# Optimization experiments

Hardware: AMD Instinct MI355X
Metric: run time of the kernel (lower is better)

## Reference

```python
import jax, jax.numpy as jnp
import numpy as np

B, S, D = 2, 2048, 2048
H, HD, RD = 16, 128, 64
ND = HD - RD  # nope head dim = 64
QR, KVR = 1536, 512  # q/kv lora ranks
EPS = 1e-6


def rmsnorm(x, w):
    return x * jax.lax.rsqrt(jnp.mean(x * x, axis=-1, keepdims=True) + EPS) * w


def rope_rotate(x, cos, sin):
    # x: [B, h, S, r]; cos/sin: [S, r/2]; pairwise complex rotation
    xr, xi = x[..., 0::2], x[..., 1::2]
    o_r = xr * cos - xi * sin
    o_i = xr * sin + xi * cos
    return jnp.stack([o_r, o_i], axis=-1).reshape(x.shape)


def setup_inputs() -> dict:
    key = jax.random.key(0)
    ks = jax.random.split(key, 12)
    sd = 0.02
    # rotary tables for rope_head_dim
    inv_freq = 1.0 / (10000.0 ** (np.arange(0, RD, 2, dtype=np.float32) / RD))
    t = np.arange(S, dtype=np.float32)
    ang = np.outer(t, inv_freq)  # [S, RD/2]
    return {
        "x": jax.random.normal(ks[0], (B, S, D), dtype=jnp.float32),
        "freqs_cos": jnp.asarray(np.cos(ang)),
        "freqs_sin": jnp.asarray(np.sin(ang)),
        "w_cq": jax.random.normal(ks[1], (QR, D), dtype=jnp.float32) * sd,
        "w_dq_nope": jax.random.normal(ks[2], (H * ND, QR), dtype=jnp.float32) * sd,
        "w_dq_rope": jax.random.normal(ks[3], (H * RD, QR), dtype=jnp.float32) * sd,
        "w_ckv": jax.random.normal(ks[4], (KVR, D), dtype=jnp.float32) * sd,
        "w_dk_nope": jax.random.normal(ks[5], (H * ND, KVR), dtype=jnp.float32) * sd,
        "w_dv": jax.random.normal(ks[6], (H * HD, KVR), dtype=jnp.float32) * sd,
        "w_krope": jax.random.normal(ks[7], (RD, D), dtype=jnp.float32) * sd,
        "w_proj": jax.random.normal(ks[8], (H * HD, H * HD), dtype=jnp.float32) * sd,
        "q_norm_w": jnp.ones((QR,), dtype=jnp.float32),
        "kv_norm_w": jnp.ones((KVR,), dtype=jnp.float32),
    }


def reference(x, freqs_cos, freqs_sin, w_cq, w_dq_nope, w_dq_rope, w_ckv,
              w_dk_nope, w_dv, w_krope, w_proj, q_norm_w, kv_norm_w):
    b, s, _ = x.shape
    # low-rank q path
    norm_q = rmsnorm(jnp.einsum("bsd,rd->bsr", x, w_cq), q_norm_w)
    q_nope = jnp.einsum("bsr,or->bso", norm_q, w_dq_nope).reshape(b, s, H, ND).transpose(0, 2, 1, 3)
    q_rope = jnp.einsum("bsr,or->bso", norm_q, w_dq_rope).reshape(b, s, H, RD).transpose(0, 2, 1, 3)
    # low-rank kv path
    norm_kv = rmsnorm(jnp.einsum("bsd,rd->bsr", x, w_ckv), kv_norm_w)
    k_nope = jnp.einsum("bsr,or->bso", norm_kv, w_dk_nope).reshape(b, s, H, ND).transpose(0, 2, 1, 3)
    v = jnp.einsum("bsr,or->bso", norm_kv, w_dv).reshape(b, s, H, HD).transpose(0, 2, 1, 3)
    # shared single-head rope key from x directly
    k_rope_raw = jnp.einsum("bsd,rd->bsr", x, w_krope).reshape(b, s, 1, RD).transpose(0, 2, 1, 3)
    # NOTE: source does `k_rope, q_rope = apply_rope(query_rope, key_rope, cis)`,
    # i.e. the rotated query lands in the K slot and the rotated (1-head) key in the Q slot.
    k_rope = rope_rotate(q_rope, freqs_cos, freqs_sin)            # [B,H,S,RD]
    q_rope_out = rope_rotate(k_rope_raw, freqs_cos, freqs_sin)     # [B,1,S,RD]
    q = jnp.concatenate([q_nope, jnp.broadcast_to(q_rope_out, (b, H, s, RD))], axis=-1)
    k = jnp.concatenate([k_nope, k_rope], axis=-1)
    # causal SDPA, scale 1/sqrt(head_dim)
    scores = jnp.einsum("bhqd,bhkd->bhqk", q, k) / jnp.sqrt(jnp.float32(HD))
    mask = jnp.tril(jnp.ones((s, s), dtype=bool))
    scores = jnp.where(mask, scores, jnp.finfo(scores.dtype).min)
    attn = jax.nn.softmax(scores, axis=-1)
    out = jnp.einsum("bhqk,bhkd->bhqd", attn, v)  # [B,H,S,HD]
    out = out.transpose(0, 2, 1, 3).reshape(b, s, H * HD)
    return jnp.einsum("bso,po->bsp", out, w_proj)
```

## Files before the change

kernel.cpp:

```cpp
#include <hip/hip_runtime.h>

typedef __attribute__((ext_vector_type(4))) float f32x4;
typedef __attribute__((ext_vector_type(8))) short short8;
typedef unsigned short ushort_t;

__device__ __forceinline__ float bf2f(ushort_t u) {
  unsigned int i = ((unsigned int)u) << 16;
  return __builtin_bit_cast(float, i);
}
__device__ __forceinline__ ushort_t f2bf(float f) {
  unsigned int x = __builtin_bit_cast(unsigned int, f);
  unsigned int r = (x + 0x7FFFu + ((x >> 16) & 1u)) >> 16;
  return (ushort_t)r;
}

__global__ __launch_bounds__(256)
void cvt_all(const float* __restrict__ x, const float* __restrict__ wcq,
             const float* __restrict__ wdqn, const float* __restrict__ wdqr,
             const float* __restrict__ wckv, const float* __restrict__ wdkn,
             const float* __restrict__ wdv, const float* __restrict__ wkr,
             const float* __restrict__ wpr,
             ushort_t* ox, ushort_t* owcq, ushort_t* owdqn, ushort_t* owdqr,
             ushort_t* owckv, ushort_t* owdkn, ushort_t* owdv, ushort_t* owkr,
             ushort_t* owpr) {
  int bid = blockIdx.x;
  const float* in; ushort_t* out;
  if (bid < 8192)       { in = x;    out = ox;    }
  else if (bid < 11264) { in = wcq;  out = owcq;  bid -= 8192;  }
  else if (bid < 12800) { in = wdqn; out = owdqn; bid -= 11264; }
  else if (bid < 14336) { in = wdqr; out = owdqr; bid -= 12800; }
  else if (bid < 15360) { in = wckv; out = owckv; bid -= 14336; }
  else if (bid < 15872) { in = wdkn; out = owdkn; bid -= 15360; }
  else if (bid < 16896) { in = wdv;  out = owdv;  bid -= 15872; }
  else if (bid < 17024) { in = wkr;  out = owkr;  bid -= 16896; }
  else                  { in = wpr;  out = owpr;  bid -= 17024; }
  const long i = ((long)bid * 256 + threadIdx.x) * 4;
  float4 v = *(const float4*)(in + i);
  ushort4 o;
  o.x = f2bf(v.x); o.y = f2bf(v.y); o.z = f2bf(v.z); o.w = f2bf(v.w);
  *(ushort4*)(out + i) = o;
}

template <int OUT_BF16>
__global__ __launch_bounds__(256)
void gemm_bt(const ushort_t* __restrict__ A, const ushort_t* __restrict__ B,
             void* __restrict__ Cv, int M, int N, int K) {
  __shared__ __align__(16) ushort_t As[128 * 64];
  __shared__ __align__(16) ushort_t Bs[128 * 64];
  const int tid = threadIdx.x;
  const int lane = tid & 63;
  const int wid = tid >> 6;
  const int m0 = blockIdx.y * 128;
  const int n0 = blockIdx.x * 128;
  const int wm = (wid >> 1) * 64;
  const int wn = (wid & 1) * 64;

  f32x4 acc[4][4];
#pragma unroll
  for (int m = 0; m < 4; ++m)
#pragma unroll
    for (int n = 0; n < 4; ++n) acc[m][n] = (f32x4){0.f, 0.f, 0.f, 0.f};

  const int ktiles = K >> 6;
  for (int kt = 0; kt < ktiles; ++kt) {
    const int k0 = kt << 6;
    __syncthreads();
#pragma unroll
    for (int i = 0; i < 4; ++i) {
      const int chunk = (i * 4 + wid) * 1024;
      const int o = chunk + lane * 16;
      const int row = o >> 7;
      const int cb = o & 127;
      const ushort_t* src = A + (long)(m0 + row) * K + (k0 + (cb >> 1));
      __builtin_amdgcn_global_load_lds((const __attribute__((address_space(1))) unsigned int*)src,
                                       (__attribute__((address_space(3))) unsigned int*)((char*)As + chunk),
                                       16, 0, 0);
    }
#pragma unroll
    for (int i = 0; i < 4; ++i) {
      const int chunk = (i * 4 + wid) * 1024;
      const int o = chunk + lane * 16;
      const int row = o >> 7;
      const int cb = o & 127;
      int brow = n0 + row;
      if (brow > N - 1) brow = N - 1;
      const ushort_t* src = B + (long)brow * K + (k0 + (cb >> 1));
      __builtin_amdgcn_global_load_lds((const __attribute__((address_space(1))) unsigned int*)src,
                                       (__attribute__((address_space(3))) unsigned int*)((char*)Bs + chunk),
                                       16, 0, 0);
    }
    __syncthreads();
#pragma unroll
    for (int kk = 0; kk < 2; ++kk) {
      const int kb = kk * 32 + ((lane >> 4) << 3);
      short8 a[4], b[4];
#pragma unroll
      for (int m = 0; m < 4; ++m)
        a[m] = *(const short8*)(As + (wm + m * 16 + (lane & 15)) * 64 + kb);
#pragma unroll
      for (int n = 0; n < 4; ++n)
        b[n] = *(const short8*)(Bs + (wn + n * 16 + (lane & 15)) * 64 + kb);
#pragma unroll
      for (int m = 0; m < 4; ++m)
#pragma unroll
        for (int n = 0; n < 4; ++n)
          acc[m][n] = __builtin_amdgcn_mfma_f32_16x16x32_bf16(a[m], b[n], acc[m][n], 0, 0, 0);
    }
  }
  const int rb = m0 + wm + ((lane >> 4) << 2);
  const int cbase = n0 + wn + (lane & 15);
#pragma unroll
  for (int m = 0; m < 4; ++m)
#pragma unroll
    for (int n = 0; n < 4; ++n) {
      const int c = cbase + n * 16;
      if (c < N) {
#pragma unroll
        for (int j = 0; j < 4; ++j) {
          const long r = rb + m * 16 + j;
          if (OUT_BF16)
            ((ushort_t*)Cv)[r * N + c] = f2bf(acc[m][n][j]);
          else
            ((float*)Cv)[r * N + c] = acc[m][n][j];
        }
      }
    }
}

__global__ __launch_bounds__(256)
void gemm_bt3(const ushort_t* __restrict__ A,
              const ushort_t* __restrict__ B0, ushort_t* __restrict__ C0, int nb0, int N0,
              const ushort_t* __restrict__ B1, ushort_t* __restrict__ C1, int nb1, int N1,
              const ushort_t* __restrict__ B2, ushort_t* __restrict__ C2, int N2,
              int K, int tvSeg) {
  __shared__ __align__(16) ushort_t S[16384];
  ushort_t* As = S;
  ushort_t* Bs = S + 8192;
  int bx = blockIdx.x;
  const ushort_t* Bp; ushort_t* Cp; int N; int seg;
  if (bx < nb0)            { Bp = B0; Cp = C0; N = N0; seg = 0; }
  else if (bx < nb0 + nb1) { Bp = B1; Cp = C1; N = N1; seg = 1; bx -= nb0; }
  else                     { Bp = B2; Cp = C2; N = N2; seg = 2; bx -= nb0 + nb1; }
  const int tid = threadIdx.x;
  const int lane = tid & 63;
  const int wid = tid >> 6;
  const int m0 = blockIdx.y * 128;
  const int n0 = bx * 128;
  const int wm = (wid >> 1) * 64;
  const int wn = (wid & 1) * 64;

  f32x4 acc[4][4];
#pragma unroll
  for (int m = 0; m < 4; ++m)
#pragma unroll
    for (int n = 0; n < 4; ++n) acc[m][n] = (f32x4){0.f, 0.f, 0.f, 0.f};

  const int ktiles = K >> 6;
  for (int kt = 0; kt < ktiles; ++kt) {
    const int k0 = kt << 6;
    __syncthreads();
#pragma unroll
    for (int i = 0; i < 4; ++i) {
      const int chunk = (i * 4 + wid) * 1024;
      const int o = chunk + lane * 16;
      const int row = o >> 7;
      const int cb = o & 127;
      const ushort_t* src = A + (long)(m0 + row) * K + (k0 + (cb >> 1));
      __builtin_amdgcn_global_load_lds((const __attribute__((address_space(1))) unsigned int*)src,
                                       (__attribute__((address_space(3))) unsigned int*)((char*)As + chunk),
                                       16, 0, 0);
    }
#pragma unroll
    for (int i = 0; i < 4; ++i) {
      const int chunk = (i * 4 + wid) * 1024;
      const int o = chunk + lane * 16;
      const int row = o >> 7;
      const int cb = o & 127;
      int brow = n0 + row;
      if (brow > N - 1) brow = N - 1;
      const ushort_t* src = Bp + (long)brow * K + (k0 + (cb >> 1));
      __builtin_amdgcn_global_load_lds((const __attribute__((address_space(1))) unsigned int*)src,
                                       (__attribute__((address_space(3))) unsigned int*)((char*)Bs + chunk),
                                       16, 0, 0);
    }
    __syncthreads();
#pragma unroll
    for (int kk = 0; kk < 2; ++kk) {
      const int kb = kk * 32 + ((lane >> 4) << 3);
      short8 a[4], b[4];
#pragma unroll
      for (int m = 0; m < 4; ++m)
        a[m] = *(const short8*)(As + (wm + m * 16 + (lane & 15)) * 64 + kb);
#pragma unroll
      for (int n = 0; n < 4; ++n)
        b[n] = *(const short8*)(Bs + (wn + n * 16 + (lane & 15)) * 64 + kb);
#pragma unroll
      for (int m = 0; m < 4; ++m)
#pragma unroll
        for (int n = 0; n < 4; ++n)
          acc[m][n] = __builtin_amdgcn_mfma_f32_16x16x32_bf16(a[m], b[n], acc[m][n], 0, 0, 0);
    }
  }
  if (seg == tvSeg) {
    __syncthreads();
    const int lrb = wm + ((lane >> 4) << 2);
    const int ldb = wn + (lane & 15);
#pragma unroll
    for (int m = 0; m < 4; ++m)
#pragma unroll
      for (int n = 0; n < 4; ++n) {
        const int ld = ldb + n * 16;
#pragma unroll
        for (int j = 0; j < 4; ++j) {
          const int lr = lrb + m * 16 + j;
          *(ushort_t*)((char*)S + lr * 256 + ((2 * ld) ^ ((lr & 15) << 4))) = f2bf(acc[m][n][j]);
        }
      }
    __syncthreads();
    const int b = m0 >> 11;
    const int s0 = m0 & 2047;
    const int bh = b * 16 + bx;
    const int d = tid & 127;
    const int sh = (tid >> 7) * 64;
#pragma unroll
    for (int i = 0; i < 8; ++i) {
      const int sbase = sh + i * 8;
      short8 val;
#pragma unroll
      for (int j = 0; j < 8; ++j) {
        const int s = sbase + j;
        val[j] = (short)*(const ushort_t*)((const char*)S + s * 256 + ((2 * d) ^ ((s & 15) << 4)));
      }
      *(short8*)(Cp + ((long)bh * 128 + d) * 2048 + s0 + sbase) = val;
    }
    return;
  }
  const int rb = m0 + wm + ((lane >> 4) << 2);
  const int cbase = n0 + wn + (lane & 15);
#pragma unroll
  for (int m = 0; m < 4; ++m)
#pragma unroll
    for (int n = 0; n < 4; ++n) {
      const int c = cbase + n * 16;
      if (c < N) {
#pragma unroll
        for (int j = 0; j < 4; ++j) {
          const long r = rb + m * 16 + j;
          Cp[r * N + c] = f2bf(acc[m][n][j]);
        }
      }
    }
}

__device__ __forceinline__ void rms_body(const ushort_t* x, const float* w,
                                         ushort_t* out, int R, float* warr) {
  const int tid = threadIdx.x;
  float ss = 0.f;
  for (int i = tid; i < R; i += 256) { float v = bf2f(x[i]); ss += v * v; }
#pragma unroll
  for (int off = 32; off; off >>= 1) ss += __shfl_xor(ss, off);
  if ((tid & 63) == 0) warr[tid >> 6] = ss;
  __syncthreads();
  const float tot = warr[0] + warr[1] + warr[2] + warr[3];
  const float rs = rsqrtf(tot / (float)R + 1e-6f);
  for (int i = tid; i < R; i += 256) out[i] = f2bf(bf2f(x[i]) * rs * w[i]);
}

__global__ __launch_bounds__(256)
void rmsnorm_both(const ushort_t* __restrict__ ckv, const float* __restrict__ kvnw,
                  ushort_t* __restrict__ nkv,
                  const ushort_t* __restrict__ cq, const float* __restrict__ qnw,
                  ushort_t* __restrict__ nq) {
  __shared__ float warr[4];
  const int bid = blockIdx.x;
  if (bid < 4096) rms_body(ckv + (long)bid * 512, kvnw, nkv + (long)bid * 512, 512, warr);
  else {
    const long row = bid - 4096;
    rms_body(cq + row * 1536, qnw, nq + row * 1536, 1536, warr);
  }
}

__device__ __forceinline__ void rope_body(const ushort_t* in, ushort_t* out,
                                          const float* fc, const float* fs,
                                          int heads, int bid) {
  const int idx = bid * 256 + threadIdx.x;
  const int i = idx & 31;
  const int rest = idx >> 5;
  const int hh = rest % heads;
  const int row = rest / heads;
  const int srow = row & 2047;
  const float c = fc[srow * 32 + i];
  const float s = fs[srow * 32 + i];
  const long base = (long)row * heads * 64 + hh * 64 + 2 * i;
  const float x0 = bf2f(in[base]);
  const float x1 = bf2f(in[base + 1]);
  out[base] = f2bf(x0 * c - x1 * s);
  out[base + 1] = f2bf(x0 * s + x1 * c);
}

__global__ __launch_bounds__(256)
void rope_kraw(const ushort_t* __restrict__ kraw, ushort_t* __restrict__ qrs,
               const float* __restrict__ fc, const float* __restrict__ fs) {
  rope_body(kraw, qrs, fc, fs, 1, blockIdx.x);
}

__global__ __launch_bounds__(256)
void rope_qr(const ushort_t* __restrict__ qr, ushort_t* __restrict__ krope,
             const float* __restrict__ fc, const float* __restrict__ fs) {
  rope_body(qr, krope, fc, fs, 16, blockIdx.x);
}

__global__ __launch_bounds__(512)
void attn_mfma(const ushort_t* __restrict__ qn, const ushort_t* __restrict__ qrs,
               const ushort_t* __restrict__ kn, const ushort_t* __restrict__ kr,
               const ushort_t* __restrict__ vt, ushort_t* __restrict__ out) {
  __shared__ __align__(16) ushort_t Ks[2][8192];
  __shared__ __align__(16) ushort_t Vts[2][8192];
  __shared__ __align__(16) ushort_t Ps[8192];
  const int tid = threadIdx.x, lane = tid & 63, wid = tid >> 6;
  const int g = lane >> 4, lq = lane & 15;
  const int bh = blockIdx.x, b = bh >> 4, h = bh & 15;
  const float scale = 0.08838834764831845f;
  char* Pbase = (char*)Ps + wid * 2048;

  auto stageK = [&](int bsel, int kt) {
    const int k0s = kt * 64;
#pragma unroll
    for (int i = 0; i < 2; ++i) {
      const int cc = wid * 2 + i;
      const int o = cc * 1024 + lane * 16;
      const int row = o >> 8;
      const int dK = ((o & 255) ^ ((row & 7) << 4)) >> 1;
      const long krow = (long)b * 2048 + k0s + row;
      const ushort_t* srcK = (dK < 64) ? (kn + krow * 1024 + h * 64 + dK)
                                       : (kr + krow * 1024 + h * 64 + (dK - 64));
      __builtin_amdgcn_global_load_lds((const __attribute__((address_space(1))) unsigned int*)srcK,
          (__attribute__((address_space(3))) unsigned int*)((char*)Ks[bsel] + cc * 1024), 16, 0, 0);
    }
  };
  auto stageV = [&](int bsel, int kt) {
    const int k0s = kt * 64;
#pragma unroll
    for (int i = 0; i < 2; ++i) {
      const int cc = wid * 2 + i;
      const int o = cc * 1024 + lane * 16;
      const int dr = o >> 7;
      const int se = ((o & 127) ^ ((dr & 7) << 4)) >> 1;
      const ushort_t* srcV = vt + ((long)bh * 128 + dr) * 2048 + k0s + se;
      __builtin_amdgcn_global_load_lds((const __attribute__((address_space(1))) unsigned int*)srcV,
          (__attribute__((address_space(3))) unsigned int*)((char*)Vts[bsel] + cc * 1024), 16, 0, 0);
    }
  };

  const int y = blockIdx.y;
  const int tq = (y < 8) ? (15 - y) : (y - 8);
  const int q0 = tq * 128;
  const int qw0 = q0 + wid * 16;
  short8 aq[4];
  {
    const long grow = (long)b * 2048 + qw0 + lq;
#pragma unroll
    for (int ks = 0; ks < 4; ++ks) {
      const int d = ks * 32 + g * 8;
      const ushort_t* src = (d < 64) ? (qn + grow * 1024 + h * 64 + d)
                                     : (qrs + grow * 64 + (d - 64));
      aq[ks] = *(const short8*)src;
    }
  }
  f32x4 oacc[8];
#pragma unroll
  for (int n = 0; n < 8; ++n) oacc[n] = (f32x4){0.f, 0.f, 0.f, 0.f};
  float sm[4] = {-3e38f, -3e38f, -3e38f, -3e38f};
  float sl[4] = {0.f, 0.f, 0.f, 0.f};

  auto qk = [&](f32x4 (&sacc)[4], int u) {
#pragma unroll
    for (int n = 0; n < 4; ++n) sacc[n] = (f32x4){0.f, 0.f, 0.f, 0.f};
    const ushort_t* Kbuf = Ks[u & 1];
    __builtin_amdgcn_s_setprio(1);
#pragma unroll
    for (int ks = 0; ks < 4; ++ks) {
      const int x = ks * 64 + g * 16;
#pragma unroll
      for (int n = 0; n < 4; ++n) {
        const int kl = n * 16 + lq;
        short8 bk = *(const short8*)((const char*)Kbuf + kl * 256 + (x ^ ((kl & 7) << 4)));
        sacc[n] = __builtin_amdgcn_mfma_f32_16x16x32_bf16(aq[ks], bk, sacc[n], 0, 0, 0);
      }
    }
    __builtin_amdgcn_s_setprio(0);
  };
  auto process = [&](f32x4 (&sacc)[4], int u) {
    const int k0 = u * 64;
    if (k0 + 63 > qw0) {
#pragma unroll
      for (int n = 0; n < 4; ++n) {
        const int key = k0 + n * 16 + lq;
#pragma unroll
        for (int j = 0; j < 4; ++j) {
          const int qrow = qw0 + g * 4 + j;
          if (key > qrow) sacc[n][j] = -3e38f;
        }
      }
    }
    float tmax[4];
#pragma unroll
    for (int j = 0; j < 4; ++j)
      tmax[j] = fmaxf(fmaxf(sacc[0][j], sacc[1][j]), fmaxf(sacc[2][j], sacc[3][j]));
#pragma unroll
    for (int off = 1; off < 16; off <<= 1)
#pragma unroll
      for (int j = 0; j < 4; ++j) tmax[j] = fmaxf(tmax[j], __shfl_xor(tmax[j], off));
    bool need = false;
#pragma unroll
    for (int j = 0; j < 4; ++j) {
      tmax[j] *= scale;
      need = need || (tmax[j] > sm[j] + 8.f);
    }
    if (__any(need)) {
#pragma unroll
      for (int j = 0; j < 4; ++j) {
        const float mn = fmaxf(sm[j], tmax[j]);
        const float fr = __expf(sm[j] - mn);
        sm[j] = mn;
        sl[j] *= fr;
#pragma unroll
        for (int n = 0; n < 8; ++n) oacc[n][j] *= fr;
      }
    }
    f32x4 p[4];
#pragma unroll
    for (int n = 0; n < 4; ++n)
#pragma unroll
      for (int j = 0; j < 4; ++j)
        p[n][j] = __expf(__builtin_fmaf(sacc[n][j], scale, -sm[j]));
    float psum[4];
#pragma unroll
    for (int j = 0; j < 4; ++j) psum[j] = p[0][j] + p[1][j] + p[2][j] + p[3][j];
#pragma unroll
    for (int off = 1; off < 16; off <<= 1)
#pragma unroll
      for (int j = 0; j < 4; ++j) psum[j] += __shfl_xor(psum[j], off);
#pragma unroll
    for (int j = 0; j < 4; ++j) sl[j] += psum[j];
#pragma unroll
    for (int n = 0; n < 4; ++n) {
      const int col2 = (n * 16 + lq) * 2;
#pragma unroll
      for (int j = 0; j < 4; ++j) {
        const int row = g * 4 + j;
        *(ushort_t*)(Pbase + row * 128 + (col2 ^ ((row & 7) << 4))) = f2bf(p[n][j]);
      }
    }
    const ushort_t* Vbuf = Vts[u & 1];
    __builtin_amdgcn_s_setprio(1);
#pragma unroll
    for (int ks2 = 0; ks2 < 2; ++ks2) {
      const int x = ks2 * 64 + g * 16;
      short8 pa = *(const short8*)(Pbase + lq * 128 + (x ^ ((lq & 7) << 4)));
#pragma unroll
      for (int nd = 0; nd < 8; ++nd) {
        const int dl = nd * 16 + lq;
        short8 vb = *(const short8*)((const char*)Vbuf + dl * 128 + (x ^ ((dl & 7) << 4)));
        oacc[nd] = __builtin_amdgcn_mfma_f32_16x16x32_bf16(pa, vb, oacc[nd], 0, 0, 0);
      }
    }
    __builtin_amdgcn_s_setprio(0);
  };

  const int kmax = 2 * tq + 2;
  f32x4 saccA[4], saccB[4];
  stageK(0, 0); stageV(0, 0); stageK(1, 1);
  asm volatile("s_waitcnt vmcnt(0)" ::: "memory");
  __builtin_amdgcn_s_barrier();
  __builtin_amdgcn_sched_barrier(0);
  qk(saccA, 0);
  for (int u = 0; u < kmax; u += 2) {
    if (u + 2 < kmax) stageK(0, u + 2);
    stageV(1, u + 1);
    qk(saccB, u + 1);
    process(saccA, u);
    asm volatile("s_waitcnt vmcnt(0)" ::: "memory");
    __builtin_amdgcn_s_barrier();
    __builtin_amdgcn_sched_barrier(0);
    if (u + 3 < kmax) stageK(1, u + 3);
    if (u + 2 < kmax) stageV(0, u + 2);
    if (u + 2 < kmax) qk(saccA, u + 2);
    process(saccB, u + 1);
    asm volatile("s_waitcnt vmcnt(0)" ::: "memory");
    __builtin_amdgcn_s_barrier();
    __builtin_amdgcn_sched_barrier(0);
  }
  float inv[4];
#pragma unroll
  for (int j = 0; j < 4; ++j) inv[j] = 1.f / sl[j];
#pragma unroll
  for (int nd = 0; nd < 8; ++nd) {
    const int d = nd * 16 + lq;
#pragma unroll
    for (int j = 0; j < 4; ++j) {
      const long row = (long)b * 2048 + qw0 + g * 4 + j;
      out[row * 2048 + h * 128 + d] = f2bf(oacc[nd][j] * inv[j]);
    }
  }
}

extern "C" void kernel_launch(void* const* d_in, const int* in_sizes, int n_in,
                              void* d_out, int out_size, void* d_ws, size_t ws_size,
                              hipStream_t stream) {
  const float* x      = (const float*)d_in[0];
  const float* fcos   = (const float*)d_in[1];
  const float* fsin   = (const float*)d_in[2];
  const float* w_cq   = (const float*)d_in[3];
  const float* w_dqn  = (const float*)d_in[4];
  const float* w_dqr  = (const float*)d_in[5];
  const float* w_ckv  = (const float*)d_in[6];
  const float* w_dkn  = (const float*)d_in[7];
  const float* w_dv   = (const float*)d_in[8];
  const float* w_kr   = (const float*)d_in[9];
  const float* w_proj = (const float*)d_in[10];
  const float* qnw    = (const float*)d_in[11];
  const float* kvnw   = (const float*)d_in[12];
  float* out = (float*)d_out;

  char* ws = (char*)d_ws;
  ushort_t* x_bf     = (ushort_t*)(ws + 0);
  ushort_t* wcq_bf   = (ushort_t*)(ws + 16777216);
  ushort_t* wdqn_bf  = (ushort_t*)(ws + 23068672);
  ushort_t* wdqr_bf  = (ushort_t*)(ws + 26214400);
  ushort_t* wckv_bf  = (ushort_t*)(ws + 29360128);
  ushort_t* wdkn_bf  = (ushort_t*)(ws + 31457280);
  ushort_t* wdv_bf   = (ushort_t*)(ws + 32505856);
  ushort_t* wpr_bf   = (ushort_t*)(ws + 34603008);
  ushort_t* cq_bf    = (ushort_t*)(ws + 42991616);
  ushort_t* krope_bf = (ushort_t*)(ws + 42991616);
  ushort_t* qrs_bf   = (ushort_t*)(ws + 51904512);
  ushort_t* ckv_bf   = (ushort_t*)(ws + 55574528);
  ushort_t* nq_bf    = (ushort_t*)(ws + 59768832);
  ushort_t* attn_bf  = (ushort_t*)(ws + 55574528);
  ushort_t* nkv_bf   = (ushort_t*)(ws + 72351744);
  ushort_t* qnope_bf = (ushort_t*)(ws + 76546048);
  ushort_t* kraw_bf  = (ushort_t*)(ws + 76546048);
  ushort_t* qr_bf    = (ushort_t*)(ws + 0);
  ushort_t* knope_bf = (ushort_t*)(ws + 8388608);
  ushort_t* wkr_bf   = (ushort_t*)(ws + 84934656);
  ushort_t* vt_bf    = (ushort_t*)(ws + 84934656);

  cvt_all<<<21120, 256, 0, stream>>>(x, w_cq, w_dqn, w_dqr, w_ckv, w_dkn, w_dv, w_kr, w_proj,
                                     x_bf, wcq_bf, wdqn_bf, wdqr_bf, wckv_bf, wdkn_bf,
                                     wdv_bf, wkr_bf, wpr_bf);
  gemm_bt3<<<dim3(17, 32), 256, 0, stream>>>(x_bf,
                                             wckv_bf, ckv_bf, 4, 512,
                                             wcq_bf, cq_bf, 12, 1536,
                                             wkr_bf, kraw_bf, 64, 2048, -1);
  rmsnorm_both<<<8192, 256, 0, stream>>>(ckv_bf, kvnw, nkv_bf, cq_bf, qnw, nq_bf);
  rope_kraw<<<512, 256, 0, stream>>>(kraw_bf, qrs_bf, fcos, fsin);
  gemm_bt3<<<dim3(16, 32), 256, 0, stream>>>(nq_bf,
                                             wdqn_bf, qnope_bf, 8, 1024,
                                             wdqr_bf, qr_bf, 8, 1024,
                                             wdqn_bf, qnope_bf, 1024, 1536, -1);
  gemm_bt3<<<dim3(24, 32), 256, 0, stream>>>(nkv_bf,
                                             wdkn_bf, knope_bf, 8, 1024,
                                             wdv_bf, vt_bf, 16, 2048,
                                             wdkn_bf, knope_bf, 1024, 512, 1);
  rope_qr<<<8192, 256, 0, stream>>>(qr_bf, krope_bf, fcos, fsin);
  attn_mfma<<<dim3(32, 16), 512, 0, stream>>>(qnope_bf, qrs_bf, knope_bf, krope_bf, vt_bf, attn_bf);
  gemm_bt<0><<<dim3(16, 32), 256, 0, stream>>>(attn_bf, wpr_bf, out, 4096, 2048, 2048);
}
```

Measured before the change: 360.2 us.

## Merge q/kv up-projection GEMMs, fuse rmsnorm with rope, pair attention q-tiles per block

```diff
diff --git a/kernel.cpp b/kernel.cpp
--- a/kernel.cpp
+++ b/kernel.cpp
@@ -132,15 +132,14 @@
               const ushort_t* __restrict__ B0, ushort_t* __restrict__ C0, int nb0, int N0,
               const ushort_t* __restrict__ B1, ushort_t* __restrict__ C1, int nb1, int N1,
               const ushort_t* __restrict__ B2, ushort_t* __restrict__ C2, int N2,
-              int K, int tvSeg) {
-  __shared__ __align__(16) ushort_t S[16384];
-  ushort_t* As = S;
-  ushort_t* Bs = S + 8192;
+              int K) {
+  __shared__ __align__(16) ushort_t As[128 * 64];
+  __shared__ __align__(16) ushort_t Bs[128 * 64];
   int bx = blockIdx.x;
-  const ushort_t* Bp; ushort_t* Cp; int N; int seg;
-  if (bx < nb0)            { Bp = B0; Cp = C0; N = N0; seg = 0; }
-  else if (bx < nb0 + nb1) { Bp = B1; Cp = C1; N = N1; seg = 1; bx -= nb0; }
-  else                     { Bp = B2; Cp = C2; N = N2; seg = 2; bx -= nb0 + nb1; }
+  const ushort_t* Bp; ushort_t* Cp; int N;
+  if (bx < nb0)            { Bp = B0; Cp = C0; N = N0; }
+  else if (bx < nb0 + nb1) { Bp = B1; Cp = C1; N = N1; bx -= nb0; }
+  else                     { Bp = B2; Cp = C2; N = N2; bx -= nb0 + nb1; }
   const int tid = threadIdx.x;
   const int lane = tid & 63;
   const int wid = tid >> 6;
@@ -201,7 +200,97 @@
           acc[m][n] = __builtin_amdgcn_mfma_f32_16x16x32_bf16(a[m], b[n], acc[m][n], 0, 0, 0);
     }
   }
-  if (seg == tvSeg) {
+  const int rb = m0 + wm + ((lane >> 4) << 2);
+  const int cbase = n0 + wn + (lane & 15);
+#pragma unroll
+  for (int m = 0; m < 4; ++m)
+#pragma unroll
+    for (int n = 0; n < 4; ++n) {
+      const int c = cbase + n * 16;
+      if (c < N) {
+#pragma unroll
+        for (int j = 0; j < 4; ++j) {
+          const long r = rb + m * 16 + j;
+          Cp[r * N + c] = f2bf(acc[m][n][j]);
+        }
+      }
+    }
+}
+
+__global__ __launch_bounds__(256)
+void gemm_qkv(const ushort_t* __restrict__ nq, const ushort_t* __restrict__ nkv,
+              const ushort_t* __restrict__ wdqn, ushort_t* __restrict__ qnope,
+              const ushort_t* __restrict__ wdqr, ushort_t* __restrict__ qr,
+              const ushort_t* __restrict__ wdkn, ushort_t* __restrict__ knope,
+              const ushort_t* __restrict__ wdv, ushort_t* __restrict__ vt) {
+  __shared__ __align__(16) ushort_t S[16384];
+  ushort_t* As = S;
+  ushort_t* Bs = S + 8192;
+  int bx = blockIdx.x;
+  const ushort_t* Ap; const ushort_t* Bp; ushort_t* Cp; int N, K; bool tv = false;
+  if (bx < 8)       { Ap = nq;  K = 1536; Bp = wdqn; Cp = qnope; N = 1024; }
+  else if (bx < 16) { Ap = nq;  K = 1536; Bp = wdqr; Cp = qr;    N = 1024; bx -= 8; }
+  else if (bx < 24) { Ap = nkv; K = 512;  Bp = wdkn; Cp = knope; N = 1024; bx -= 16; }
+  else              { Ap = nkv; K = 512;  Bp = wdv;  Cp = vt;    N = 2048; bx -= 24; tv = true; }
+  const int tid = threadIdx.x;
+  const int lane = tid & 63;
+  const int wid = tid >> 6;
+  const int m0 = blockIdx.y * 128;
+  const int n0 = bx * 128;
+  const int wm = (wid >> 1) * 64;
+  const int wn = (wid & 1) * 64;
+
+  f32x4 acc[4][4];
+#pragma unroll
+  for (int m = 0; m < 4; ++m)
+#pragma unroll
+    for (int n = 0; n < 4; ++n) acc[m][n] = (f32x4){0.f, 0.f, 0.f, 0.f};
+
+  const int ktiles = K >> 6;
+  for (int kt = 0; kt < ktiles; ++kt) {
+    const int k0 = kt << 6;
+    __syncthreads();
+#pragma unroll
+    for (int i = 0; i < 4; ++i) {
+      const int chunk = (i * 4 + wid) * 1024;
+      const int o = chunk + lane * 16;
+      const int row = o >> 7;
+      const int cb = o & 127;
+      const ushort_t* src = Ap + (long)(m0 + row) * K + (k0 + (cb >> 1));
+      __builtin_amdgcn_global_load_lds((const __attribute__((address_space(1))) unsigned int*)src,
+                                       (__attribute__((address_space(3))) unsigned int*)((char*)As + chunk),
+                                       16, 0, 0);
+    }
+#pragma unroll
+    for (int i = 0; i < 4; ++i) {
+      const int chunk = (i * 4 + wid) * 1024;
+      const int o = chunk + lane * 16;
+      const int row = o >> 7;
+      const int cb = o & 127;
+      const ushort_t* src = Bp + (long)(n0 + row) * K + (k0 + (cb >> 1));
+      __builtin_amdgcn_global_load_lds((const __attribute__((address_space(1))) unsigned int*)src,
+                                       (__attribute__((address_space(3))) unsigned int*)((char*)Bs + chunk),
+                                       16, 0, 0);
+    }
+    __syncthreads();
+#pragma unroll
+    for (int kk = 0; kk < 2; ++kk) {
+      const int kb = kk * 32 + ((lane >> 4) << 3);
+      short8 a[4], b[4];
+#pragma unroll
+      for (int m = 0; m < 4; ++m)
+        a[m] = *(const short8*)(As + (wm + m * 16 + (lane & 15)) * 64 + kb);
+#pragma unroll
+      for (int n = 0; n < 4; ++n)
+        b[n] = *(const short8*)(Bs + (wn + n * 16 + (lane & 15)) * 64 + kb);
+#pragma unroll
+      for (int m = 0; m < 4; ++m)
+#pragma unroll
+        for (int n = 0; n < 4; ++n)
+          acc[m][n] = __builtin_amdgcn_mfma_f32_16x16x32_bf16(a[m], b[n], acc[m][n], 0, 0, 0);
+    }
+  }
+  if (tv) {
     __syncthreads();
     const int lrb = wm + ((lane >> 4) << 2);
     const int ldb = wn + (lane & 15);
@@ -242,12 +331,10 @@
 #pragma unroll
     for (int n = 0; n < 4; ++n) {
       const int c = cbase + n * 16;
-      if (c < N) {
-#pragma unroll
-        for (int j = 0; j < 4; ++j) {
-          const long r = rb + m * 16 + j;
-          Cp[r * N + c] = f2bf(acc[m][n][j]);
-        }
+#pragma unroll
+      for (int j = 0; j < 4; ++j) {
+        const long r = rb + m * 16 + j;
+        Cp[r * N + c] = f2bf(acc[m][n][j]);
       }
     }
 }
@@ -264,20 +351,6 @@
   const float tot = warr[0] + warr[1] + warr[2] + warr[3];
   const float rs = rsqrtf(tot / (float)R + 1e-6f);
   for (int i = tid; i < R; i += 256) out[i] = f2bf(bf2f(x[i]) * rs * w[i]);
-}
-
-__global__ __launch_bounds__(256)
-void rmsnorm_both(const ushort_t* __restrict__ ckv, const float* __restrict__ kvnw,
-                  ushort_t* __restrict__ nkv,
-                  const ushort_t* __restrict__ cq, const float* __restrict__ qnw,
-                  ushort_t* __restrict__ nq) {
-  __shared__ float warr[4];
-  const int bid = blockIdx.x;
-  if (bid < 4096) rms_body(ckv + (long)bid * 512, kvnw, nkv + (long)bid * 512, 512, warr);
-  else {
-    const long row = bid - 4096;
-    rms_body(cq + row * 1536, qnw, nq + row * 1536, 1536, warr);
-  }
 }
 
 __device__ __forceinline__ void rope_body(const ushort_t* in, ushort_t* out,
@@ -299,9 +372,21 @@
 }
 
 __global__ __launch_bounds__(256)
-void rope_kraw(const ushort_t* __restrict__ kraw, ushort_t* __restrict__ qrs,
-               const float* __restrict__ fc, const float* __restrict__ fs) {
-  rope_body(kraw, qrs, fc, fs, 1, blockIdx.x);
+void rms_rope(const ushort_t* __restrict__ ckv, const float* __restrict__ kvnw,
+              ushort_t* __restrict__ nkv,
+              const ushort_t* __restrict__ cq, const float* __restrict__ qnw,
+              ushort_t* __restrict__ nq,
+              const ushort_t* __restrict__ kraw, ushort_t* __restrict__ qrs,
+              const float* __restrict__ fc, const float* __restrict__ fs) {
+  __shared__ float warr[4];
+  const int bid = blockIdx.x;
+  if (bid < 4096) rms_body(ckv + (long)bid * 512, kvnw, nkv + (long)bid * 512, 512, warr);
+  else if (bid < 8192) {
+    const long row = bid - 4096;
+    rms_body(cq + row * 1536, qnw, nq + row * 1536, 1536, warr);
+  } else {
+    rope_body(kraw, qrs, fc, fs, 1, bid - 8192);
+  }
 }
 
 __global__ __launch_bounds__(256)
@@ -352,155 +437,157 @@
     }
   };
 
-  const int y = blockIdx.y;
-  const int tq = (y < 8) ? (15 - y) : (y - 8);
-  const int q0 = tq * 128;
-  const int qw0 = q0 + wid * 16;
-  short8 aq[4];
-  {
-    const long grow = (long)b * 2048 + qw0 + lq;
-#pragma unroll
-    for (int ks = 0; ks < 4; ++ks) {
-      const int d = ks * 32 + g * 8;
-      const ushort_t* src = (d < 64) ? (qn + grow * 1024 + h * 64 + d)
-                                     : (qrs + grow * 64 + (d - 64));
-      aq[ks] = *(const short8*)src;
-    }
-  }
-  f32x4 oacc[8];
-#pragma unroll
-  for (int n = 0; n < 8; ++n) oacc[n] = (f32x4){0.f, 0.f, 0.f, 0.f};
-  float sm[4] = {-3e38f, -3e38f, -3e38f, -3e38f};
-  float sl[4] = {0.f, 0.f, 0.f, 0.f};
-
-  auto qk = [&](f32x4 (&sacc)[4], int u) {
-#pragma unroll
-    for (int n = 0; n < 4; ++n) sacc[n] = (f32x4){0.f, 0.f, 0.f, 0.f};
-    const ushort_t* Kbuf = Ks[u & 1];
-    __builtin_amdgcn_s_setprio(1);
-#pragma unroll
-    for (int ks = 0; ks < 4; ++ks) {
-      const int x = ks * 64 + g * 16;
+  const int pair = blockIdx.y;
+  for (int half = 0; half < 2; ++half) {
+    const int tq = half ? (15 - pair) : pair;
+    const int q0 = tq * 128;
+    const int qw0 = q0 + wid * 16;
+    short8 aq[4];
+    {
+      const long grow = (long)b * 2048 + qw0 + lq;
+#pragma unroll
+      for (int ks = 0; ks < 4; ++ks) {
+        const int d = ks * 32 + g * 8;
+        const ushort_t* src = (d < 64) ? (qn + grow * 1024 + h * 64 + d)
+                                       : (qrs + grow * 64 + (d - 64));
+        aq[ks] = *(const short8*)src;
+      }
+    }
+    f32x4 oacc[8];
+#pragma unroll
+    for (int n = 0; n < 8; ++n) oacc[n] = (f32x4){0.f, 0.f, 0.f, 0.f};
+    float sm[4] = {-3e38f, -3e38f, -3e38f, -3e38f};
+    float sl[4] = {0.f, 0.f, 0.f, 0.f};
+
+    auto qk = [&](f32x4 (&sacc)[4], int u) {
+#pragma unroll
+      for (int n = 0; n < 4; ++n) sacc[n] = (f32x4){0.f, 0.f, 0.f, 0.f};
+      const ushort_t* Kbuf = Ks[u & 1];
+      __builtin_amdgcn_s_setprio(1);
+#pragma unroll
+      for (int ks = 0; ks < 4; ++ks) {
+        const int x = ks * 64 + g * 16;
+#pragma unroll
+        for (int n = 0; n < 4; ++n) {
+          const int kl = n * 16 + lq;
+          short8 bk = *(const short8*)((const char*)Kbuf + kl * 256 + (x ^ ((kl & 7) << 4)));
+          sacc[n] = __builtin_amdgcn_mfma_f32_16x16x32_bf16(aq[ks], bk, sacc[n], 0, 0, 0);
+        }
+      }
+      __builtin_amdgcn_s_setprio(0);
+    };
+    auto process = [&](f32x4 (&sacc)[4], int u) {
+      const int k0 = u * 64;
+      if (k0 + 63 > qw0) {
+#pragma unroll
+        for (int n = 0; n < 4; ++n) {
+          const int key = k0 + n * 16 + lq;
+#pragma unroll
+          for (int j = 0; j < 4; ++j) {
+            const int qrow = qw0 + g * 4 + j;
+            if (key > qrow) sacc[n][j] = -3e38f;
+          }
+        }
+      }
+      float tmax[4];
+#pragma unroll
+      for (int j = 0; j < 4; ++j)
+        tmax[j] = fmaxf(fmaxf(sacc[0][j], sacc[1][j]), fmaxf(sacc[2][j], sacc[3][j]));
+#pragma unroll
+      for (int off = 1; off < 16; off <<= 1)
+#pragma unroll
+        for (int j = 0; j < 4; ++j) tmax[j] = fmaxf(tmax[j], __shfl_xor(tmax[j], off));
+      bool need = false;
+#pragma unroll
+      for (int j = 0; j < 4; ++j) {
+        tmax[j] *= scale;
+        need = need || (tmax[j] > sm[j] + 8.f);
+      }
+      if (__any(need)) {
+#pragma unroll
+        for (int j = 0; j < 4; ++j) {
+          const float mn = fmaxf(sm[j], tmax[j]);
+          const float fr = __expf(sm[j] - mn);
+          sm[j] = mn;
+          sl[j] *= fr;
+#pragma unroll
+          for (int n = 0; n < 8; ++n) oacc[n][j] *= fr;
+        }
+      }
+      f32x4 p[4];
+#pragma unroll
+      for (int n = 0; n < 4; ++n)
+#pragma unroll
+        for (int j = 0; j < 4; ++j)
+          p[n][j] = __expf(__builtin_fmaf(sacc[n][j], scale, -sm[j]));
+      float psum[4];
+#pragma unroll
+      for (int j = 0; j < 4; ++j) psum[j] = p[0][j] + p[1][j] + p[2][j] + p[3][j];
+#pragma unroll
+      for (int off = 1; off < 16; off <<= 1)
+#pragma unroll
+        for (int j = 0; j < 4; ++j) psum[j] += __shfl_xor(psum[j], off);
+#pragma unroll
+      for (int j = 0; j < 4; ++j) sl[j] += psum[j];
 #pragma unroll
       for (int n = 0; n < 4; ++n) {
-        const int kl = n * 16 + lq;
-        short8 bk = *(const short8*)((const char*)Kbuf + kl * 256 + (x ^ ((kl & 7) << 4)));
-        sacc[n] = __builtin_amdgcn_mfma_f32_16x16x32_bf16(aq[ks], bk, sacc[n], 0, 0, 0);
-      }
-    }
-    __builtin_amdgcn_s_setprio(0);
-  };
-  auto process = [&](f32x4 (&sacc)[4], int u) {
-    const int k0 = u * 64;
-    if (k0 + 63 > qw0) {
-#pragma unroll
-      for (int n = 0; n < 4; ++n) {
-        const int key = k0 + n * 16 + lq;
+        const int col2 = (n * 16 + lq) * 2;
 #pragma unroll
         for (int j = 0; j < 4; ++j) {
-          const int qrow = qw0 + g * 4 + j;
-          if (key > qrow) sacc[n][j] = -3e38f;
-        }
-      }
-    }
-    float tmax[4];
-#pragma unroll
-    for (int j = 0; j < 4; ++j)
-      tmax[j] = fmaxf(fmaxf(sacc[0][j], sacc[1][j]), fmaxf(sacc[2][j], sacc[3][j]));
-#pragma unroll
-    for (int off = 1; off < 16; off <<= 1)
-#pragma unroll
-      for (int j = 0; j < 4; ++j) tmax[j] = fmaxf(tmax[j], __shfl_xor(tmax[j], off));
-    bool need = false;
-#pragma unroll
-    for (int j = 0; j < 4; ++j) {
-      tmax[j] *= scale;
-      need = need || (tmax[j] > sm[j] + 8.f);
-    }
-    if (__any(need)) {
-#pragma unroll
-      for (int j = 0; j < 4; ++j) {
-        const float mn = fmaxf(sm[j], tmax[j]);
-        const float fr = __expf(sm[j] - mn);
-        sm[j] = mn;
-        sl[j] *= fr;
-#pragma unroll
-        for (int n = 0; n < 8; ++n) oacc[n][j] *= fr;
-      }
-    }
-    f32x4 p[4];
-#pragma unroll
-    for (int n = 0; n < 4; ++n)
-#pragma unroll
-      for (int j = 0; j < 4; ++j)
-        p[n][j] = __expf(__builtin_fmaf(sacc[n][j], scale, -sm[j]));
-    float psum[4];
-#pragma unroll
-    for (int j = 0; j < 4; ++j) psum[j] = p[0][j] + p[1][j] + p[2][j] + p[3][j];
-#pragma unroll
-    for (int off = 1; off < 16; off <<= 1)
-#pragma unroll
-      for (int j = 0; j < 4; ++j) psum[j] += __shfl_xor(psum[j], off);
-#pragma unroll
-    for (int j = 0; j < 4; ++j) sl[j] += psum[j];
-#pragma unroll
-    for (int n = 0; n < 4; ++n) {
-      const int col2 = (n * 16 + lq) * 2;
-#pragma unroll
-      for (int j = 0; j < 4; ++j) {
-        const int row = g * 4 + j;
-        *(ushort_t*)(Pbase + row * 128 + (col2 ^ ((row & 7) << 4))) = f2bf(p[n][j]);
-      }
-    }
-    const ushort_t* Vbuf = Vts[u & 1];
-    __builtin_amdgcn_s_setprio(1);
-#pragma unroll
-    for (int ks2 = 0; ks2 < 2; ++ks2) {
-      const int x = ks2 * 64 + g * 16;
-      short8 pa = *(const short8*)(Pbase + lq * 128 + (x ^ ((lq & 7) << 4)));
-#pragma unroll
-      for (int nd = 0; nd < 8; ++nd) {
-        const int dl = nd * 16 + lq;
-        short8 vb = *(const short8*)((const char*)Vbuf + dl * 128 + (x ^ ((dl & 7) << 4)));
-        oacc[nd] = __builtin_amdgcn_mfma_f32_16x16x32_bf16(pa, vb, oacc[nd], 0, 0, 0);
-      }
-    }
-    __builtin_amdgcn_s_setprio(0);
-  };
-
-  const int kmax = 2 * tq + 2;
-  f32x4 saccA[4], saccB[4];
-  stageK(0, 0); stageV(0, 0); stageK(1, 1);
-  asm volatile("s_waitcnt vmcnt(0)" ::: "memory");
-  __builtin_amdgcn_s_barrier();
-  __builtin_amdgcn_sched_barrier(0);
-  qk(saccA, 0);
-  for (int u = 0; u < kmax; u += 2) {
-    if (u + 2 < kmax) stageK(0, u + 2);
-    stageV(1, u + 1);
-    qk(saccB, u + 1);
-    process(saccA, u);
+          const int row = g * 4 + j;
+          *(ushort_t*)(Pbase + row * 128 + (col2 ^ ((row & 7) << 4))) = f2bf(p[n][j]);
+        }
+      }
+      const ushort_t* Vbuf = Vts[u & 1];
+      __builtin_amdgcn_s_setprio(1);
+#pragma unroll
+      for (int ks2 = 0; ks2 < 2; ++ks2) {
+        const int x = ks2 * 64 + g * 16;
+        short8 pa = *(const short8*)(Pbase + lq * 128 + (x ^ ((lq & 7) << 4)));
+#pragma unroll
+        for (int nd = 0; nd < 8; ++nd) {
+          const int dl = nd * 16 + lq;
+          short8 vb = *(const short8*)((const char*)Vbuf + dl * 128 + (x ^ ((dl & 7) << 4)));
+          oacc[nd] = __builtin_amdgcn_mfma_f32_16x16x32_bf16(pa, vb, oacc[nd], 0, 0, 0);
+        }
+      }
+      __builtin_amdgcn_s_setprio(0);
+    };
+
+    const int kmax = 2 * tq + 2;
+    f32x4 saccA[4], saccB[4];
+    stageK(0, 0); stageV(0, 0); stageK(1, 1);
     asm volatile("s_waitcnt vmcnt(0)" ::: "memory");
     __builtin_amdgcn_s_barrier();
     __builtin_amdgcn_sched_barrier(0);
-    if (u + 3 < kmax) stageK(1, u + 3);
-    if (u + 2 < kmax) stageV(0, u + 2);
-    if (u + 2 < kmax) qk(saccA, u + 2);
-    process(saccB, u + 1);
-    asm volatile("s_waitcnt vmcnt(0)" ::: "memory");
-    __builtin_amdgcn_s_barrier();
-    __builtin_amdgcn_sched_barrier(0);
-  }
-  float inv[4];
-#pragma unroll
-  for (int j = 0; j < 4; ++j) inv[j] = 1.f / sl[j];
-#pragma unroll
-  for (int nd = 0; nd < 8; ++nd) {
-    const int d = nd * 16 + lq;
-#pragma unroll
-    for (int j = 0; j < 4; ++j) {
-      const long row = (long)b * 2048 + qw0 + g * 4 + j;
-      out[row * 2048 + h * 128 + d] = f2bf(oacc[nd][j] * inv[j]);
+    qk(saccA, 0);
+    for (int u = 0; u < kmax; u += 2) {
+      if (u + 2 < kmax) stageK(0, u + 2);
+      stageV(1, u + 1);
+      qk(saccB, u + 1);
+      process(saccA, u);
+      asm volatile("s_waitcnt vmcnt(0)" ::: "memory");
+      __builtin_amdgcn_s_barrier();
+      __builtin_amdgcn_sched_barrier(0);
+      if (u + 3 < kmax) stageK(1, u + 3);
+      if (u + 2 < kmax) stageV(0, u + 2);
+      if (u + 2 < kmax) qk(saccA, u + 2);
+      process(saccB, u + 1);
+      asm volatile("s_waitcnt vmcnt(0)" ::: "memory");
+      __builtin_amdgcn_s_barrier();
+      __builtin_amdgcn_sched_barrier(0);
+    }
+    float inv[4];
+#pragma unroll
+    for (int j = 0; j < 4; ++j) inv[j] = 1.f / sl[j];
+#pragma unroll
+    for (int nd = 0; nd < 8; ++nd) {
+      const int d = nd * 16 + lq;
+#pragma unroll
+      for (int j = 0; j < 4; ++j) {
+        const long row = (long)b * 2048 + qw0 + g * 4 + j;
+        out[row * 2048 + h * 128 + d] = f2bf(oacc[nd][j] * inv[j]);
+      }
     }
   }
 }
@@ -526,6 +613,7 @@
   char* ws = (char*)d_ws;
   ushort_t* x_bf     = (ushort_t*)(ws + 0);
   ushort_t* wcq_bf   = (ushort_t*)(ws + 16777216);
+  ushort_t* qrs_bf   = (ushort_t*)(ws + 16777216);
   ushort_t* wdqn_bf  = (ushort_t*)(ws + 23068672);
   ushort_t* wdqr_bf  = (ushort_t*)(ws + 26214400);
   ushort_t* wckv_bf  = (ushort_t*)(ws + 29360128);
@@ -534,7 +622,6 @@
   ushort_t* wpr_bf   = (ushort_t*)(ws + 34603008);
   ushort_t* cq_bf    = (ushort_t*)(ws + 42991616);
   ushort_t* krope_bf = (ushort_t*)(ws + 42991616);
-  ushort_t* qrs_bf   = (ushort_t*)(ws + 51904512);
   ushort_t* ckv_bf   = (ushort_t*)(ws + 55574528);
   ushort_t* nq_bf    = (ushort_t*)(ws + 59768832);
   ushort_t* attn_bf  = (ushort_t*)(ws + 55574528);
@@ -552,18 +639,15 @@
   gemm_bt3<<<dim3(17, 32), 256, 0, stream>>>(x_bf,
                                              wckv_bf, ckv_bf, 4, 512,
                                              wcq_bf, cq_bf, 12, 1536,
-                                             wkr_bf, kraw_bf, 64, 2048, -1);
-  rmsnorm_both<<<8192, 256, 0, stream>>>(ckv_bf, kvnw, nkv_bf, cq_bf, qnw, nq_bf);
-  rope_kraw<<<512, 256, 0, stream>>>(kraw_bf, qrs_bf, fcos, fsin);
-  gemm_bt3<<<dim3(16, 32), 256, 0, stream>>>(nq_bf,
-                                             wdqn_bf, qnope_bf, 8, 1024,
-                                             wdqr_bf, qr_bf, 8, 1024,
-                                             wdqn_bf, qnope_bf, 1024, 1536, -1);
-  gemm_bt3<<<dim3(24, 32), 256, 0, stream>>>(nkv_bf,
-                                             wdkn_bf, knope_bf, 8, 1024,
-                                             wdv_bf, vt_bf, 16, 2048,
-                                             wdkn_bf, knope_bf, 1024, 512, 1);
+                                             wkr_bf, kraw_bf, 64, 2048);
+  rms_rope<<<8704, 256, 0, stream>>>(ckv_bf, kvnw, nkv_bf, cq_bf, qnw, nq_bf,
+                                     kraw_bf, qrs_bf, fcos, fsin);
+  gemm_qkv<<<dim3(40, 32), 256, 0, stream>>>(nq_bf, nkv_bf,
+                                             wdqn_bf, qnope_bf,
+                                             wdqr_bf, qr_bf,
+                                             wdkn_bf, knope_bf,
+                                             wdv_bf, vt_bf);
   rope_qr<<<8192, 256, 0, stream>>>(qr_bf, krope_bf, fcos, fsin);
-  attn_mfma<<<dim3(32, 16), 512, 0, stream>>>(qnope_bf, qrs_bf, knope_bf, krope_bf, vt_bf, attn_bf);
+  attn_mfma<<<dim3(32, 8), 512, 0, stream>>>(qnope_bf, qrs_bf, knope_bf, krope_bf, vt_bf, attn_bf);
   gemm_bt<0><<<dim3(16, 32), 256, 0, stream>>>(attn_bf, wpr_bf, out, 4096, 2048, 2048);
 }
```

Result: faster. 340.6 us (-5.5%).
